# Optimization experiments

Measured on AMD Instinct MI355X. Metric: run time of the kernel, lower is better.

## Reference

```python
import jax, jax.numpy as jnp
import numpy as np

E = 1024   # embed_dim
H = 16     # num_heads
D = E // H # head_dim
T, N, M, B = 1024, 1024, 1023, 4  # tgt len, leaves, tree nodes, batch


def setup_inputs() -> dict:
    key0 = jax.random.key(0)
    ks = jax.random.split(key0, 8)
    s = 1.0 / np.sqrt(E).astype(np.float32)  # xavier-ish scale
    return {
        "query": jax.random.normal(ks[0], (T, B, E), jnp.float32),
        "key": jax.random.normal(ks[1], (N, B, E), jnp.float32),
        "node_key": jax.random.normal(ks[2], (M, B, E), jnp.float32),
        "in_proj_weight": jax.random.normal(ks[3], (3 * E, E), jnp.float32) * s,
        "in_proj_bias": jnp.zeros((3 * E,), jnp.float32),
        "out_w": jax.random.normal(ks[4], (E, E), jnp.float32) * s,
        "out_b": jnp.zeros((E,), jnp.float32),
        "dw_w": jax.random.normal(ks[5], (H, E), jnp.float32) * s,
        "dw_b": jnp.zeros((H,), jnp.float32),
        "key_padding_mask": jnp.zeros((B, N), bool),
        "node_padding_mask": jnp.zeros((B, M), bool),
    }


def reference(query, key, node_key, in_proj_weight, in_proj_bias,
              out_w, out_b, dw_w, dw_b, key_padding_mask, node_padding_mask):
    t, b, e = query.shape
    n, m = key.shape[0], node_key.shape[0]
    d = e // H
    scaling = d ** -0.5
    # fused in-proj slices (F.linear: y = x W^T + bias)
    Wq, Wk, Wv = in_proj_weight[:e], in_proj_weight[e:2 * e], in_proj_weight[2 * e:]
    bq, bk, bv = in_proj_bias[:e], in_proj_bias[e:2 * e], in_proj_bias[2 * e:]
    q = (query @ Wq.T + bq) * scaling
    k = key @ Wk.T + bk
    v = key @ Wv.T + bv
    nk = node_key @ Wk.T + bk          # node_kv_same: nodes share kv projection
    nv = node_key @ Wv.T + bv

    def heads(x, L):  # [L,B,E] -> [B,H,L,D]
        return x.reshape(L, b, H, d).transpose(1, 2, 0, 3)

    qh, kh, vh = heads(q, t), heads(k, n), heads(v, n)
    nkh, nvh = heads(nk, m), heads(nv, m)

    # per-head affinity weights for merged stack nodes (dwstack, sigmoid act)
    dw = jax.nn.sigmoid(node_key @ dw_w.T + dw_b)   # [M,B,H]
    nvh = nvh * dw.transpose(1, 2, 0)[..., None]    # weighted node values

    s_leaf = jnp.einsum('bhtd,bhnd->bhtn', qh, kh)
    s_node = jnp.einsum('bhtd,bhmd->bhtm', qh, nkh)
    neg = jnp.finfo(s_leaf.dtype).min
    s_leaf = jnp.where(key_padding_mask[:, None, None, :], neg, s_leaf)
    s_node = jnp.where(node_padding_mask[:, None, None, :], neg, s_node)

    attn = jax.nn.softmax(jnp.concatenate([s_leaf, s_node], axis=-1), axis=-1)
    vals = jnp.concatenate([vh, nvh], axis=2)       # [B,H,N+M,D]
    o = jnp.einsum('bhts,bhsd->bhtd', attn, vals)   # [B,H,T,D]
    o = o.transpose(2, 0, 1, 3).reshape(t, b, e)
    return o @ out_w.T + out_b
```

## Files before the change

kernel.cpp:

```cpp
#include <hip/hip_runtime.h>
#include <cstdint>
#include <cstddef>

using short8 = __attribute__((ext_vector_type(8))) short;
using f32x4  = __attribute__((ext_vector_type(4))) float;

constexpr int T_ = 1024;
constexpr int N_ = 1024;
constexpr int M_ = 1023;
constexpr int B_ = 4;
constexpr int E_ = 1024;
constexpr int H_ = 16;
constexpr int D_ = 64;

#define MFMA16(a, b, c) __builtin_amdgcn_mfma_f32_16x16x32_bf16((a), (b), (c), 0, 0, 0)

__device__ __forceinline__ unsigned short f2bf(float f) {
    unsigned int u = __float_as_uint(f);
    u += 0x7FFF + ((u >> 16) & 1);
    return (unsigned short)(u >> 16);
}
__device__ __forceinline__ float bf2f(unsigned short s) {
    return __uint_as_float(((unsigned int)s) << 16);
}

__device__ __forceinline__ unsigned int cvt_pk_bf16(float lo, float hi) {
    unsigned int r;
    asm("v_cvt_pk_bf16_f32 %0, %1, %2" : "=v"(r) : "v"(lo), "v"(hi));
    return r;
}

typedef __attribute__((address_space(1))) const unsigned char gc_byte;
typedef __attribute__((address_space(3))) unsigned char lds_byte;
__device__ __forceinline__ void gload16(const void* g, void* lds) {
    __builtin_amdgcn_global_load_lds((gc_byte*)(uintptr_t)g,
                                     (lds_byte*)(unsigned int)(uintptr_t)lds,
                                     16, 0, 0);
}

__device__ __forceinline__ void conv_body(const float* __restrict__ src,
                                          unsigned short* __restrict__ dst,
                                          int i, int n)
{
    if (i + 4 <= n) {
        const float4 v = *reinterpret_cast<const float4*>(src + i);
        ushort4 o;
        o.x = f2bf(v.x); o.y = f2bf(v.y); o.z = f2bf(v.z); o.w = f2bf(v.w);
        *reinterpret_cast<ushort4*>(dst + i) = o;
    } else {
        for (int k = 0; k < 4; ++k)
            dst[i + k] = (i + k < n) ? f2bf(src[i + k]) : (unsigned short)0;
    }
}

__global__ void conv_all(const float* __restrict__ query,
                         const float* __restrict__ key,
                         const float* __restrict__ node_key,
                         const float* __restrict__ ipw,
                         const float* __restrict__ out_w,
                         unsigned short* __restrict__ xq,
                         unsigned short* __restrict__ xk,
                         unsigned short* __restrict__ xn,
                         unsigned short* __restrict__ wbf,
                         unsigned short* __restrict__ wohi,
                         unsigned short* __restrict__ wolo)
{
    const int blk = blockIdx.x;
    const int tid = threadIdx.x;
    if (blk < 4096) {
        conv_body(query, xq, (blk * 256 + tid) * 4, 4194304);
    } else if (blk < 8192) {
        conv_body(key, xk, ((blk - 4096) * 256 + tid) * 4, 4194304);
    } else if (blk < 12288) {
        conv_body(node_key, xn, ((blk - 8192) * 256 + tid) * 4, 4190208);
    } else if (blk < 15360) {
        conv_body(ipw, wbf, ((blk - 12288) * 256 + tid) * 4, 3145728);
    } else {
        const int i = ((blk - 15360) * 256 + tid) * 4;
        const float4 v = *reinterpret_cast<const float4*>(out_w + i);
        float a[4] = {v.x, v.y, v.z, v.w};
        ushort4 hi, lo;
        unsigned short h[4], l[4];
        #pragma unroll
        for (int k = 0; k < 4; ++k) {
            h[k] = f2bf(a[k]);
            l[k] = f2bf(a[k] - bf2f(h[k]));
        }
        hi.x = h[0]; hi.y = h[1]; hi.z = h[2]; hi.w = h[3];
        lo.x = l[0]; lo.y = l[1]; lo.z = l[2]; lo.w = l[3];
        *reinterpret_cast<ushort4*>(wohi + i) = hi;
        *reinterpret_cast<ushort4*>(wolo + i) = lo;
    }
}

__global__ void dw_kernel(const float* __restrict__ node_key,
                          const float* __restrict__ dw_w,
                          const float* __restrict__ dw_b,
                          float* __restrict__ dwb)
{
    __shared__ float rowbuf[E_];
    const int r = blockIdx.x;
    const int tid = threadIdx.x;
    for (int idx = tid; idx < E_; idx += 256)
        rowbuf[idx] = node_key[(size_t)r * E_ + idx];
    __syncthreads();
    const int h = tid >> 4;
    const int lane = tid & 15;
    float acc = 0.f;
    const float* wrow = dw_w + (size_t)h * E_;
    for (int k = lane; k < E_; k += 16)
        acc = fmaf(rowbuf[k], wrow[k], acc);
    acc += __shfl_xor(acc, 8);
    acc += __shfl_xor(acc, 4);
    acc += __shfl_xor(acc, 2);
    acc += __shfl_xor(acc, 1);
    if (lane == 0) {
        float x = acc + dw_b[h];
        dwb[(size_t)r * H_ + h] = 1.f / (1.f + __expf(-x));
    }
}

__global__ __launch_bounds__(256) void proj_mfma(
    const unsigned short* __restrict__ xq,
    const unsigned short* __restrict__ xk,
    const unsigned short* __restrict__ xn,
    const unsigned short* __restrict__ wbf,
    const float* __restrict__ ipb,
    const float* __restrict__ dwb,
    unsigned short* __restrict__ qb,
    unsigned short* __restrict__ kb,
    unsigned short* __restrict__ vtb,
    unsigned short* __restrict__ nkb,
    unsigned short* __restrict__ nvtb)
{
    __shared__ unsigned short LDS[3][2][128 * 32];

    const unsigned short* A;
    const unsigned short* W;
    const float* bias;
    const float* dwm = nullptr;
    unsigned short* out;
    int epi;
    float scale = 1.f;
    switch (blockIdx.z) {
      case 0:  A = xq; W = wbf;           bias = ipb;        out = qb;   epi = 1; scale = 0.18033688011112042f; break;
      case 1:  A = xk; W = wbf + 1048576; bias = ipb + 1024; out = kb;   epi = 1; break;
      case 2:  A = xk; W = wbf + 2097152; bias = ipb + 2048; out = vtb;  epi = 2; break;
      case 3:  A = xn; W = wbf + 1048576; bias = ipb + 1024; out = nkb;  epi = 1; break;
      default: A = xn; W = wbf + 2097152; bias = ipb + 2048; out = nvtb; epi = 2; dwm = dwb; break;
    }

    const int tid = threadIdx.x;
    const int l = tid & 63, w = tid >> 6;
    const int brow = blockIdx.y * 128;
    const int bcol = blockIdx.x * 128;

    const int ch0 = w * 64 + l;
    const int ch1 = 256 + w * 64 + l;
    const int u0 = ((ch0 & 3) ^ ((ch0 >> 3) & 3)) * 8;
    const int u1 = ((ch1 & 3) ^ ((ch1 >> 3) & 3)) * 8;
    const unsigned short* gA0 = A + (size_t)(brow + (ch0 >> 2)) * E_ + u0;
    const unsigned short* gA1 = A + (size_t)(brow + (ch1 >> 2)) * E_ + u1;
    const unsigned short* gW0 = W + (size_t)(bcol + (ch0 >> 2)) * E_ + u0;
    const unsigned short* gW1 = W + (size_t)(bcol + (ch1 >> 2)) * E_ + u1;

    auto STAGE = [&](int buf, int kt) {
        gload16(gA0 + kt, &LDS[buf][0][(size_t)w * 512]);
        gload16(gA1 + kt, &LDS[buf][0][(size_t)(4 + w) * 512]);
        gload16(gW0 + kt, &LDS[buf][1][(size_t)w * 512]);
        gload16(gW1 + kt, &LDS[buf][1][(size_t)(4 + w) * 512]);
    };

    f32x4 acc[4][4];
    #pragma unroll
    for (int m = 0; m < 4; ++m)
        #pragma unroll
        for (int n = 0; n < 4; ++n)
            acc[m][n] = (f32x4){0.f, 0.f, 0.f, 0.f};

    const int wr = (w >> 1) * 64, wc = (w & 1) * 64;
    const int fr = l & 15;
    const int ko = (((l >> 4) ^ ((fr >> 1) & 3))) * 8;

    STAGE(0, 0);
    STAGE(1, 32);

    for (int t = 0; t < 32; ++t) {
        if (t < 31) asm volatile("s_waitcnt vmcnt(4)" ::: "memory");
        else        asm volatile("s_waitcnt vmcnt(0)" ::: "memory");
        __builtin_amdgcn_sched_barrier(0);
        __builtin_amdgcn_s_barrier();
        __builtin_amdgcn_sched_barrier(0);

        if (t < 30) STAGE((t + 2) % 3, (t + 2) * 32);

        const int cur = t % 3;
        short8 av[4], bv[4];
        #pragma unroll
        for (int m = 0; m < 4; ++m)
            av[m] = *reinterpret_cast<const short8*>(&LDS[cur][0][(wr + m * 16 + fr) * 32 + ko]);
        #pragma unroll
        for (int n = 0; n < 4; ++n)
            bv[n] = *reinterpret_cast<const short8*>(&LDS[cur][1][(wc + n * 16 + fr) * 32 + ko]);
        __builtin_amdgcn_s_setprio(1);
        #pragma unroll
        for (int m = 0; m < 4; ++m)
            #pragma unroll
            for (int n = 0; n < 4; ++n)
                acc[m][n] = MFMA16(av[m], bv[n], acc[m][n]);
        __builtin_amdgcn_s_setprio(0);
    }

    #pragma unroll
    for (int n = 0; n < 4; ++n) {
        const int c = bcol + wc + n * 16 + fr;
        const float bi = bias[c];
        #pragma unroll
        for (int m = 0; m < 4; ++m) {
            #pragma unroll
            for (int j = 0; j < 4; ++j) {
                const int r = brow + wr + m * 16 + (l >> 4) * 4 + j;
                float v = (acc[m][n][j] + bi) * scale;
                const int rn = r >> 2, b = r & 3, hh = c >> 6, dd = c & 63;
                if (epi == 1) {
                    out[((size_t)(b * H_ + hh) * 1024 + rn) * 64 + dd] = f2bf(v);
                } else {
                    if (dwm) v *= dwm[(size_t)r * H_ + hh];
                    out[(((size_t)(b * H_ + hh) * 32 + (rn >> 5)) * 64 + dd) * 32 + (rn & 31)] = f2bf(v);
                }
            }
        }
    }
}

__global__ __launch_bounds__(256) void outproj_mfma(
    const unsigned short* __restrict__ ahi,
    const unsigned short* __restrict__ alo,
    const unsigned short* __restrict__ whi,
    const unsigned short* __restrict__ wlo,
    const float* __restrict__ out_b,
    float* __restrict__ out)
{
    __shared__ unsigned short LDS[2][4][128 * 32];

    const int tid = threadIdx.x;
    const int l = tid & 63, w = tid >> 6;
    const int brow = blockIdx.y * 128;
    const int bcol = blockIdx.x * 128;

    const int ch0 = w * 64 + l;
    const int ch1 = 256 + w * 64 + l;
    const int u0 = ((ch0 & 3) ^ ((ch0 >> 3) & 3)) * 8;
    const int u1 = ((ch1 & 3) ^ ((ch1 >> 3) & 3)) * 8;
    const size_t ra0 = (size_t)(brow + (ch0 >> 2)) * E_ + u0;
    const size_t ra1 = (size_t)(brow + (ch1 >> 2)) * E_ + u1;
    const size_t rb0 = (size_t)(bcol + (ch0 >> 2)) * E_ + u0;
    const size_t rb1 = (size_t)(bcol + (ch1 >> 2)) * E_ + u1;

    auto STAGE = [&](int buf, int kt) {
        gload16(ahi + ra0 + kt, &LDS[buf][0][(size_t)w * 512]);
        gload16(ahi + ra1 + kt, &LDS[buf][0][(size_t)(4 + w) * 512]);
        gload16(alo + ra0 + kt, &LDS[buf][1][(size_t)w * 512]);
        gload16(alo + ra1 + kt, &LDS[buf][1][(size_t)(4 + w) * 512]);
        gload16(whi + rb0 + kt, &LDS[buf][2][(size_t)w * 512]);
        gload16(whi + rb1 + kt, &LDS[buf][2][(size_t)(4 + w) * 512]);
        gload16(wlo + rb0 + kt, &LDS[buf][3][(size_t)w * 512]);
        gload16(wlo + rb1 + kt, &LDS[buf][3][(size_t)(4 + w) * 512]);
    };

    f32x4 acc[4][4];
    #pragma unroll
    for (int m = 0; m < 4; ++m)
        #pragma unroll
        for (int n = 0; n < 4; ++n)
            acc[m][n] = (f32x4){0.f, 0.f, 0.f, 0.f};

    const int wr = (w >> 1) * 64, wc = (w & 1) * 64;
    const int fr = l & 15;
    const int ko = (((l >> 4) ^ ((fr >> 1) & 3))) * 8;

    STAGE(0, 0);
    __syncthreads();
    for (int t = 0; t < 32; ++t) {
        const int cur = t & 1;
        if (t < 31) STAGE(cur ^ 1, (t + 1) * 32);
        short8 ah[4], al[4], bh[4], bl[4];
        #pragma unroll
        for (int m = 0; m < 4; ++m) {
            ah[m] = *reinterpret_cast<const short8*>(&LDS[cur][0][(wr + m * 16 + fr) * 32 + ko]);
            al[m] = *reinterpret_cast<const short8*>(&LDS[cur][1][(wr + m * 16 + fr) * 32 + ko]);
        }
        #pragma unroll
        for (int n = 0; n < 4; ++n) {
            bh[n] = *reinterpret_cast<const short8*>(&LDS[cur][2][(wc + n * 16 + fr) * 32 + ko]);
            bl[n] = *reinterpret_cast<const short8*>(&LDS[cur][3][(wc + n * 16 + fr) * 32 + ko]);
        }
        #pragma unroll
        for (int m = 0; m < 4; ++m)
            #pragma unroll
            for (int n = 0; n < 4; ++n) {
                acc[m][n] = MFMA16(ah[m], bh[n], acc[m][n]);
                acc[m][n] = MFMA16(al[m], bh[n], acc[m][n]);
                acc[m][n] = MFMA16(ah[m], bl[n], acc[m][n]);
            }
        if (t < 31) __syncthreads();
    }

    #pragma unroll
    for (int n = 0; n < 4; ++n) {
        const int c = bcol + wc + n * 16 + fr;
        const float bi = out_b[c];
        #pragma unroll
        for (int m = 0; m < 4; ++m)
            #pragma unroll
            for (int j = 0; j < 4; ++j) {
                const int r = brow + wr + m * 16 + (l >> 4) * 4 + j;
                out[(size_t)r * E_ + c] = acc[m][n][j] + bi;
            }
    }
}

__global__ __launch_bounds__(256) void attn_mfma(
    const unsigned short* __restrict__ qbf,
    const unsigned short* __restrict__ kbf,
    const unsigned short* __restrict__ nkbf,
    const unsigned short* __restrict__ vtb,
    const unsigned short* __restrict__ nvtb,
    const unsigned char* __restrict__ kpm,
    const unsigned char* __restrict__ npm,
    float* __restrict__ pacc,
    float* __restrict__ pm,
    float* __restrict__ pl)
{
    __shared__ unsigned short Kl[2][64 * 64];
    __shared__ unsigned short Vl[2][64 * 64];
    __shared__ float maskF[1024];
    __shared__ int tmask[16];

    const int tid = threadIdx.x;
    const int l = tid & 63, w = tid >> 6;
    const int bh = blockIdx.x, b = bh >> 4;
    const int t0 = blockIdx.y * 64;
    const int half = blockIdx.z;

    const unsigned short* kb_ = half ? nkbf : kbf;
    const unsigned short* vb_ = half ? nvtb : vtb;

    if (tid < 16) tmask[tid] = 0;
    __syncthreads();
    for (int s = tid; s < 1024; s += 256) {
        int masked;
        if (half == 0) masked = kpm[(size_t)b * N_ + s] ? 1 : 0;
        else           masked = (s < M_ && !npm[(size_t)b * M_ + s]) ? 0 : 1;
        maskF[s] = masked ? -60000.f : 0.f;
        if (masked) atomicOr(&tmask[s >> 6], 1);
    }

    auto STAGE = [&](int buf, int s0) {
        #pragma unroll
        for (int u = 0; u < 2; ++u) {
            const int c = u * 256 + tid;
            const int krow = c >> 3;
            const int kcol = ((c & 7) * 16) ^ ((krow & 7) << 4);
            gload16((const unsigned char*)kb_ +
                        ((size_t)(bh * 1024 + s0 + krow) * 64) * 2 + kcol,
                    (unsigned char*)&Kl[buf][0] + c * 16);
            const int kg = c >> 6;
            const int dd = c & 63;
            const int kv = s0 + kg * 8;
            const int kp = kv >> 5;
            gload16((const unsigned char*)vb_ +
                        (((size_t)(bh * 32 + kp) * 64 + dd) * 32 + (kv & 31)) * 2,
                    (unsigned char*)&Vl[buf][0] + c * 16);
        }
    };

    const int g = l >> 4;
    const int q = l & 15;

    const int qrow = t0 + w * 16 + q;
    const short8 aq0 = *reinterpret_cast<const short8*>(&qbf[((size_t)bh * T_ + qrow) * 64 + g * 8]);
    const short8 aq1 = *reinterpret_cast<const short8*>(&qbf[((size_t)bh * T_ + qrow) * 64 + 32 + g * 8]);

    float mold = -30000.f, lr = 0.f;
    f32x4 acco[4];
    #pragma unroll
    for (int n = 0; n < 4; ++n) acco[n] = (f32x4){0.f, 0.f, 0.f, 0.f};

    const int ksw = (l & 7) << 4;
    const int kb0 = q * 128 + ((g * 16) ^ ksw);
    const int kb1 = q * 128 + ((64 + g * 16) ^ ksw);
    const int vb0 = g * 1024 + q * 16;

    const int src0 = (g & 1) * 32 + q;
    const int src1 = src0 + 16;
    const bool selhi = (l & 32) != 0;

    STAGE(0, 0);
    __syncthreads();

    for (int it = 0; it < 16; ++it) {
        const int s0 = it * 64;
        const int cur = it & 1;
        if (it < 15) STAGE(cur ^ 1, s0 + 64);

        const unsigned char* const Kc = (const unsigned char*)&Kl[cur][0];
        const unsigned char* const Vc = (const unsigned char*)&Vl[cur][0];

        f32x4 accs[4];
        #pragma unroll
        for (int n = 0; n < 4; ++n) accs[n] = (f32x4){0.f, 0.f, 0.f, 0.f};
        __builtin_amdgcn_s_setprio(1);
        #pragma unroll
        for (int n = 0; n < 4; ++n) {
            const short8 k0 = *reinterpret_cast<const short8*>(Kc + n * 2048 + kb0);
            const short8 k1 = *reinterpret_cast<const short8*>(Kc + n * 2048 + kb1);
            accs[n] = MFMA16(k0, aq0, accs[n]);
            accs[n] = MFMA16(k1, aq1, accs[n]);
        }
        __builtin_amdgcn_s_setprio(0);

        if (tmask[s0 >> 6]) {
            #pragma unroll
            for (int n = 0; n < 4; ++n) {
                const float4 mz = *reinterpret_cast<const float4*>(&maskF[s0 + n * 16 + g * 4]);
                accs[n][0] += mz.x;
                accs[n][1] += mz.y;
                accs[n][2] += mz.z;
                accs[n][3] += mz.w;
            }
        }

        float mx = -60000.f;
        #pragma unroll
        for (int n = 0; n < 4; ++n)
            #pragma unroll
            for (int j = 0; j < 4; ++j) mx = fmaxf(mx, accs[n][j]);
        mx = fmaxf(mx, __shfl_xor(mx, 16));
        mx = fmaxf(mx, __shfl_xor(mx, 32));

        if (__any(mx > mold + 8.f)) {
            const float mn = fmaxf(mold, mx);
            const float f = __builtin_amdgcn_exp2f(mold - mn);
            mold = mn;
            lr *= f;
            #pragma unroll
            for (int n = 0; n < 4; ++n)
                #pragma unroll
                for (int j = 0; j < 4; ++j) acco[n][j] *= f;
        }

        float p[4][4];
        float ps = 0.f;
        #pragma unroll
        for (int n = 0; n < 4; ++n)
            #pragma unroll
            for (int j = 0; j < 4; ++j) {
                p[n][j] = __builtin_amdgcn_exp2f(accs[n][j] - mold);
                ps += p[n][j];
            }
        ps += __shfl_xor(ps, 16);
        ps += __shfl_xor(ps, 32);
        lr += ps;

        unsigned int ppk[4][2];
        #pragma unroll
        for (int n = 0; n < 4; ++n) {
            ppk[n][0] = cvt_pk_bf16(p[n][0], p[n][1]);
            ppk[n][1] = cvt_pk_bf16(p[n][2], p[n][3]);
        }

        union UF { int4 i4; short8 s8; } pf[2];
        #pragma unroll
        for (int h = 0; h < 2; ++h) {
            const unsigned int a0 = __shfl((int)ppk[2 * h][0],     src0);
            const unsigned int b0 = __shfl((int)ppk[2 * h + 1][0], src0);
            const unsigned int a1 = __shfl((int)ppk[2 * h][1],     src0);
            const unsigned int b1 = __shfl((int)ppk[2 * h + 1][1], src0);
            const unsigned int a2 = __shfl((int)ppk[2 * h][0],     src1);
            const unsigned int b2 = __shfl((int)ppk[2 * h + 1][0], src1);
            const unsigned int a3 = __shfl((int)ppk[2 * h][1],     src1);
            const unsigned int b3 = __shfl((int)ppk[2 * h + 1][1], src1);
            pf[h].i4.x = selhi ? b0 : a0;
            pf[h].i4.y = selhi ? b1 : a1;
            pf[h].i4.z = selhi ? b2 : a2;
            pf[h].i4.w = selhi ? b3 : a3;
        }

        __builtin_amdgcn_s_setprio(1);
        #pragma unroll
        for (int n = 0; n < 4; ++n) {
            const short8 v0 = *reinterpret_cast<const short8*>(Vc + n * 256 + vb0);
            const short8 v1 = *reinterpret_cast<const short8*>(Vc + 4096 + n * 256 + vb0);
            acco[n] = MFMA16(v0, pf[0].s8, acco[n]);
            acco[n] = MFMA16(v1, pf[1].s8, acco[n]);
        }
        __builtin_amdgcn_s_setprio(0);

        __syncthreads();
    }

    const size_t row = ((size_t)(half * 64 + bh)) * 1024 + t0 + w * 16 + q;
    #pragma unroll
    for (int n = 0; n < 4; ++n) {
        float4 st;
        st.x = acco[n][0];
        st.y = acco[n][1];
        st.z = acco[n][2];
        st.w = acco[n][3];
        *reinterpret_cast<float4*>(&pacc[row * 64 + n * 16 + g * 4]) = st;
    }
    if (l < 16) {
        pm[row] = mold;
        pl[row] = lr;
    }
}

__global__ void merge_kernel(const float* __restrict__ pacc,
                             const float* __restrict__ pm,
                             const float* __restrict__ pl,
                             unsigned short* __restrict__ ohi,
                             unsigned short* __restrict__ olo)
{
    const int g = blockIdx.x * 256 + threadIdx.x;
    const int row = g >> 4;
    const int d4 = (g & 15) * 4;
    const int bh = row >> 10, t = row & 1023;
    const int b = bh >> 4, h = bh & 15;

    const float m0 = pm[row], m1 = pm[65536 + row];
    const float l0 = pl[row], l1 = pl[65536 + row];
    const float ms = fmaxf(m0, m1);
    const float w0 = __builtin_amdgcn_exp2f(m0 - ms);
    const float w1 = __builtin_amdgcn_exp2f(m1 - ms);
    const float den = 1.f / (l0 * w0 + l1 * w1);

    const float4 a0 = *reinterpret_cast<const float4*>(&pacc[(size_t)row * 64 + d4]);
    const float4 a1 = *reinterpret_cast<const float4*>(&pacc[(size_t)(65536 + row) * 64 + d4]);

    float o[4] = {
        (a0.x * w0 + a1.x * w1) * den,
        (a0.y * w0 + a1.y * w1) * den,
        (a0.z * w0 + a1.z * w1) * den,
        (a0.w * w0 + a1.w * w1) * den,
    };
    ushort4 vh_, vl_;
    unsigned short hh[4], ll[4];
    #pragma unroll
    for (int k = 0; k < 4; ++k) {
        hh[k] = f2bf(o[k]);
        ll[k] = f2bf(o[k] - bf2f(hh[k]));
    }
    vh_.x = hh[0]; vh_.y = hh[1]; vh_.z = hh[2]; vh_.w = hh[3];
    vl_.x = ll[0]; vl_.y = ll[1]; vl_.z = ll[2]; vl_.w = ll[3];
    const size_t oidx = ((size_t)t * B_ + b) * E_ + h * D_ + d4;
    *reinterpret_cast<ushort4*>(&ohi[oidx]) = vh_;
    *reinterpret_cast<ushort4*>(&olo[oidx]) = vl_;
}

extern "C" void kernel_launch(void* const* d_in, const int* in_sizes, int n_in,
                              void* d_out, int out_size, void* d_ws, size_t ws_size,
                              hipStream_t stream) {
    const float* query    = (const float*)d_in[0];
    const float* key      = (const float*)d_in[1];
    const float* node_key = (const float*)d_in[2];
    const float* ipw      = (const float*)d_in[3];
    const float* ipb      = (const float*)d_in[4];
    const float* out_w    = (const float*)d_in[5];
    const float* out_b    = (const float*)d_in[6];
    const float* dw_w     = (const float*)d_in[7];
    const float* dw_b     = (const float*)d_in[8];
    const unsigned char* kpm = (const unsigned char*)d_in[9];
    const unsigned char* npm = (const unsigned char*)d_in[10];
    float* out = (float*)d_out;

    char* p = (char*)d_ws;
    auto alloc = [&](size_t bytes) {
        char* r = p;
        p += (bytes + 255) & ~(size_t)255;
        return r;
    };
    unsigned short* xq    = (unsigned short*)alloc((size_t)4096 * 1024 * 2);
    unsigned short* xk    = (unsigned short*)alloc((size_t)4096 * 1024 * 2);
    unsigned short* xn    = (unsigned short*)alloc((size_t)4096 * 1024 * 2);
    unsigned short* wbf   = (unsigned short*)alloc((size_t)3072 * 1024 * 2);
    (void)alloc((size_t)2 * 1024 * 1024);
    unsigned short* wohi  = (unsigned short*)alloc((size_t)1024 * 1024 * 2);
    unsigned short* wolo  = (unsigned short*)alloc((size_t)1024 * 1024 * 2);
    unsigned short* qb    = (unsigned short*)alloc((size_t)64 * 1024 * 64 * 2);
    unsigned short* kb_   = (unsigned short*)alloc((size_t)64 * 1024 * 64 * 2);
    unsigned short* nkb   = (unsigned short*)alloc((size_t)64 * 1024 * 64 * 2);
    unsigned short* vtb   = (unsigned short*)alloc((size_t)64 * 1024 * 64 * 2);
    unsigned short* nvtb  = (unsigned short*)alloc((size_t)64 * 1024 * 64 * 2);
    unsigned short* ohi   = (unsigned short*)alloc((size_t)4096 * 1024 * 2);
    unsigned short* olo   = (unsigned short*)alloc((size_t)4096 * 1024 * 2);
    float*          dwb   = (float*)alloc((size_t)4096 * 16 * 4);
    float*          pm    = (float*)alloc((size_t)2 * 65536 * 4);
    float*          pl    = (float*)alloc((size_t)2 * 65536 * 4);
    float*          pacc  = (float*)xq;

    const dim3 blk(256);

    conv_all<<<dim3(16384), blk, 0, stream>>>(query, key, node_key, ipw, out_w,
                                              xq, xk, xn, wbf, wohi, wolo);

    dw_kernel<<<dim3(M_ * B_), blk, 0, stream>>>(node_key, dw_w, dw_b, dwb);

    proj_mfma<<<dim3(8, 32, 5), blk, 0, stream>>>(xq, xk, xn, wbf, ipb, dwb,
                                                  qb, kb_, vtb, nkb, nvtb);

    attn_mfma<<<dim3(64, 16, 2), blk, 0, stream>>>(qb, kb_, nkb, vtb, nvtb,
                                                   kpm, npm, pacc, pm, pl);

    merge_kernel<<<dim3(4096), blk, 0, stream>>>(pacc, pm, pl, ohi, olo);

    outproj_mfma<<<dim3(8, 32), blk, 0, stream>>>(ohi, olo, wohi, wolo, out_b, out);
}
```

Baseline: 254.0 us.

## Fuse leaf and node attention halves into one pass, dropping merge kernel

The attention kernel now walks all 2048 keys (leaves then nodes) in one online-softmax loop per block, instead of splitting them across two blocks and combining partials in a separate merge kernel. It normalizes the output and writes the hi/lo bf16 split directly, removing the partial accumulator/max/sum round-trip through global memory and one launch. The cost is half as many attention blocks (1024 instead of 2048), each with a loop twice as long, so there is less parallelism per CU. The mask table is also stored as bf16 in shared memory to save space.

```diff
diff --git a/kernel.cpp b/kernel.cpp
--- a/kernel.cpp
+++ b/kernel.cpp
@@ -328,48 +328,54 @@
     const unsigned short* __restrict__ nvtb,
     const unsigned char* __restrict__ kpm,
     const unsigned char* __restrict__ npm,
-    float* __restrict__ pacc,
-    float* __restrict__ pm,
-    float* __restrict__ pl)
+    unsigned short* __restrict__ ohi,
+    unsigned short* __restrict__ olo)
 {
     __shared__ unsigned short Kl[2][64 * 64];
     __shared__ unsigned short Vl[2][64 * 64];
-    __shared__ float maskF[1024];
-    __shared__ int tmask[16];
+    __shared__ unsigned short maskB[2048];
+    __shared__ int tmask[32];
 
     const int tid = threadIdx.x;
     const int l = tid & 63, w = tid >> 6;
-    const int bh = blockIdx.x, b = bh >> 4;
+    const int bh = blockIdx.x, b = bh >> 4, h = bh & 15;
     const int t0 = blockIdx.y * 64;
-    const int half = blockIdx.z;
-
-    const unsigned short* kb_ = half ? nkbf : kbf;
-    const unsigned short* vb_ = half ? nvtb : vtb;
-
-    if (tid < 16) tmask[tid] = 0;
+
+    if (tid < 32) tmask[tid] = 0;
     __syncthreads();
-    for (int s = tid; s < 1024; s += 256) {
-        int masked;
-        if (half == 0) masked = kpm[(size_t)b * N_ + s] ? 1 : 0;
-        else           masked = (s < M_ && !npm[(size_t)b * M_ + s]) ? 0 : 1;
-        maskF[s] = masked ? -60000.f : 0.f;
-        if (masked) atomicOr(&tmask[s >> 6], 1);
+    {
+        const unsigned short negbf = f2bf(-60000.f);
+        for (int s = tid; s < 2048; s += 256) {
+            int masked;
+            if (s < N_) masked = kpm[(size_t)b * N_ + s] ? 1 : 0;
+            else {
+                const int m = s - N_;
+                masked = (m < M_ && !npm[(size_t)b * M_ + m]) ? 0 : 1;
+            }
+            maskB[s] = masked ? negbf : (unsigned short)0;
+            if (masked) atomicOr(&tmask[s >> 6], 1);
+        }
     }
 
     auto STAGE = [&](int buf, int s0) {
+        const unsigned short* ksrc;
+        const unsigned short* vsrc;
+        int srow;
+        if (s0 < N_) { ksrc = kbf;  vsrc = vtb;  srow = s0; }
+        else         { ksrc = nkbf; vsrc = nvtb; srow = s0 - N_; }
         #pragma unroll
         for (int u = 0; u < 2; ++u) {
             const int c = u * 256 + tid;
             const int krow = c >> 3;
             const int kcol = ((c & 7) * 16) ^ ((krow & 7) << 4);
-            gload16((const unsigned char*)kb_ +
-                        ((size_t)(bh * 1024 + s0 + krow) * 64) * 2 + kcol,
+            gload16((const unsigned char*)ksrc +
+                        ((size_t)(bh * 1024 + srow + krow) * 64) * 2 + kcol,
                     (unsigned char*)&Kl[buf][0] + c * 16);
             const int kg = c >> 6;
             const int dd = c & 63;
-            const int kv = s0 + kg * 8;
+            const int kv = srow + kg * 8;
             const int kp = kv >> 5;
-            gload16((const unsigned char*)vb_ +
+            gload16((const unsigned char*)vsrc +
                         (((size_t)(bh * 32 + kp) * 64 + dd) * 32 + (kv & 31)) * 2,
                     (unsigned char*)&Vl[buf][0] + c * 16);
         }
@@ -399,10 +405,10 @@
     STAGE(0, 0);
     __syncthreads();
 
-    for (int it = 0; it < 16; ++it) {
+    for (int it = 0; it < 32; ++it) {
         const int s0 = it * 64;
         const int cur = it & 1;
-        if (it < 15) STAGE(cur ^ 1, s0 + 64);
+        if (it < 31) STAGE(cur ^ 1, s0 + 64);
 
         const unsigned char* const Kc = (const unsigned char*)&Kl[cur][0];
         const unsigned char* const Vc = (const unsigned char*)&Vl[cur][0];
@@ -423,11 +429,9 @@
         if (tmask[s0 >> 6]) {
             #pragma unroll
             for (int n = 0; n < 4; ++n) {
-                const float4 mz = *reinterpret_cast<const float4*>(&maskF[s0 + n * 16 + g * 4]);
-                accs[n][0] += mz.x;
-                accs[n][1] += mz.y;
-                accs[n][2] += mz.z;
-                accs[n][3] += mz.w;
+                #pragma unroll
+                for (int j = 0; j < 4; ++j)
+                    accs[n][j] += bf2f(maskB[s0 + n * 16 + g * 4 + j]);
             }
         }
 
@@ -472,19 +476,19 @@
 
         union UF { int4 i4; short8 s8; } pf[2];
         #pragma unroll
-        for (int h = 0; h < 2; ++h) {
-            const unsigned int a0 = __shfl((int)ppk[2 * h][0],     src0);
-            const unsigned int b0 = __shfl((int)ppk[2 * h + 1][0], src0);
-            const unsigned int a1 = __shfl((int)ppk[2 * h][1],     src0);
-            const unsigned int b1 = __shfl((int)ppk[2 * h + 1][1], src0);
-            const unsigned int a2 = __shfl((int)ppk[2 * h][0],     src1);
-            const unsigned int b2 = __shfl((int)ppk[2 * h + 1][0], src1);
-            const unsigned int a3 = __shfl((int)ppk[2 * h][1],     src1);
-            const unsigned int b3 = __shfl((int)ppk[2 * h + 1][1], src1);
-            pf[h].i4.x = selhi ? b0 : a0;
-            pf[h].i4.y = selhi ? b1 : a1;
-            pf[h].i4.z = selhi ? b2 : a2;
-            pf[h].i4.w = selhi ? b3 : a3;
+        for (int hh2 = 0; hh2 < 2; ++hh2) {
+            const unsigned int a0 = __shfl((int)ppk[2 * hh2][0],     src0);
+            const unsigned int b0 = __shfl((int)ppk[2 * hh2 + 1][0], src0);
+            const unsigned int a1 = __shfl((int)ppk[2 * hh2][1],     src0);
+            const unsigned int b1 = __shfl((int)ppk[2 * hh2 + 1][1], src0);
+            const unsigned int a2 = __shfl((int)ppk[2 * hh2][0],     src1);
+            const unsigned int b2 = __shfl((int)ppk[2 * hh2 + 1][0], src1);
+            const unsigned int a3 = __shfl((int)ppk[2 * hh2][1],     src1);
+            const unsigned int b3 = __shfl((int)ppk[2 * hh2 + 1][1], src1);
+            pf[hh2].i4.x = selhi ? b0 : a0;
+            pf[hh2].i4.y = selhi ? b1 : a1;
+            pf[hh2].i4.z = selhi ? b2 : a2;
+            pf[hh2].i4.w = selhi ? b3 : a3;
         }
 
         __builtin_amdgcn_s_setprio(1);
@@ -500,62 +504,25 @@
         __syncthreads();
     }
 
-    const size_t row = ((size_t)(half * 64 + bh)) * 1024 + t0 + w * 16 + q;
+    const float linv = 1.f / lr;
+    const int t = t0 + w * 16 + q;
+    const size_t obase = ((size_t)t * B_ + b) * E_ + h * 64;
     #pragma unroll
     for (int n = 0; n < 4; ++n) {
-        float4 st;
-        st.x = acco[n][0];
-        st.y = acco[n][1];
-        st.z = acco[n][2];
-        st.w = acco[n][3];
-        *reinterpret_cast<float4*>(&pacc[row * 64 + n * 16 + g * 4]) = st;
-    }
-    if (l < 16) {
-        pm[row] = mold;
-        pl[row] = lr;
-    }
-}
-
-__global__ void merge_kernel(const float* __restrict__ pacc,
-                             const float* __restrict__ pm,
-                             const float* __restrict__ pl,
-                             unsigned short* __restrict__ ohi,
-                             unsigned short* __restrict__ olo)
-{
-    const int g = blockIdx.x * 256 + threadIdx.x;
-    const int row = g >> 4;
-    const int d4 = (g & 15) * 4;
-    const int bh = row >> 10, t = row & 1023;
-    const int b = bh >> 4, h = bh & 15;
-
-    const float m0 = pm[row], m1 = pm[65536 + row];
-    const float l0 = pl[row], l1 = pl[65536 + row];
-    const float ms = fmaxf(m0, m1);
-    const float w0 = __builtin_amdgcn_exp2f(m0 - ms);
-    const float w1 = __builtin_amdgcn_exp2f(m1 - ms);
-    const float den = 1.f / (l0 * w0 + l1 * w1);
-
-    const float4 a0 = *reinterpret_cast<const float4*>(&pacc[(size_t)row * 64 + d4]);
-    const float4 a1 = *reinterpret_cast<const float4*>(&pacc[(size_t)(65536 + row) * 64 + d4]);
-
-    float o[4] = {
-        (a0.x * w0 + a1.x * w1) * den,
-        (a0.y * w0 + a1.y * w1) * den,
-        (a0.z * w0 + a1.z * w1) * den,
-        (a0.w * w0 + a1.w * w1) * den,
-    };
-    ushort4 vh_, vl_;
-    unsigned short hh[4], ll[4];
-    #pragma unroll
-    for (int k = 0; k < 4; ++k) {
-        hh[k] = f2bf(o[k]);
-        ll[k] = f2bf(o[k] - bf2f(hh[k]));
-    }
-    vh_.x = hh[0]; vh_.y = hh[1]; vh_.z = hh[2]; vh_.w = hh[3];
-    vl_.x = ll[0]; vl_.y = ll[1]; vl_.z = ll[2]; vl_.w = ll[3];
-    const size_t oidx = ((size_t)t * B_ + b) * E_ + h * D_ + d4;
-    *reinterpret_cast<ushort4*>(&ohi[oidx]) = vh_;
-    *reinterpret_cast<ushort4*>(&olo[oidx]) = vl_;
+        ushort4 h4, l4;
+        unsigned short hv[4], lv[4];
+        #pragma unroll
+        for (int j = 0; j < 4; ++j) {
+            const float v = acco[n][j] * linv;
+            hv[j] = f2bf(v);
+            lv[j] = f2bf(v - bf2f(hv[j]));
+        }
+        h4.x = hv[0]; h4.y = hv[1]; h4.z = hv[2]; h4.w = hv[3];
+        l4.x = lv[0]; l4.y = lv[1]; l4.z = lv[2]; l4.w = lv[3];
+        const size_t oidx = obase + n * 16 + g * 4;
+        *reinterpret_cast<ushort4*>(&ohi[oidx]) = h4;
+        *reinterpret_cast<ushort4*>(&olo[oidx]) = l4;
+    }
 }
 
 extern "C" void kernel_launch(void* const* d_in, const int* in_sizes, int n_in,
@@ -584,7 +551,6 @@
     unsigned short* xk    = (unsigned short*)alloc((size_t)4096 * 1024 * 2);
     unsigned short* xn    = (unsigned short*)alloc((size_t)4096 * 1024 * 2);
     unsigned short* wbf   = (unsigned short*)alloc((size_t)3072 * 1024 * 2);
-    (void)alloc((size_t)2 * 1024 * 1024);
     unsigned short* wohi  = (unsigned short*)alloc((size_t)1024 * 1024 * 2);
     unsigned short* wolo  = (unsigned short*)alloc((size_t)1024 * 1024 * 2);
     unsigned short* qb    = (unsigned short*)alloc((size_t)64 * 1024 * 64 * 2);
@@ -595,9 +561,6 @@
     unsigned short* ohi   = (unsigned short*)alloc((size_t)4096 * 1024 * 2);
     unsigned short* olo   = (unsigned short*)alloc((size_t)4096 * 1024 * 2);
     float*          dwb   = (float*)alloc((size_t)4096 * 16 * 4);
-    float*          pm    = (float*)alloc((size_t)2 * 65536 * 4);
-    float*          pl    = (float*)alloc((size_t)2 * 65536 * 4);
-    float*          pacc  = (float*)xq;
 
     const dim3 blk(256);
 
@@ -609,10 +572,8 @@
     proj_mfma<<<dim3(8, 32, 5), blk, 0, stream>>>(xq, xk, xn, wbf, ipb, dwb,
                                                   qb, kb_, vtb, nkb, nvtb);
 
-    attn_mfma<<<dim3(64, 16, 2), blk, 0, stream>>>(qb, kb_, nkb, vtb, nvtb,
-                                                   kpm, npm, pacc, pm, pl);
-
-    merge_kernel<<<dim3(4096), blk, 0, stream>>>(pacc, pm, pl, ohi, olo);
+    attn_mfma<<<dim3(64, 16), blk, 0, stream>>>(qb, kb_, nkb, vtb, nvtb,
+                                                kpm, npm, ohi, olo);
 
     outproj_mfma<<<dim3(8, 32), blk, 0, stream>>>(ohi, olo, wohi, wolo, out_b, out);
 }
```

Result: faster. 247.1 us (-2.7%).
